# Performance work log

Measured on AMD Instinct MI355X. Metric: run time of the kernel, lower is better.

The kernel has to match this reference:

```python
import jax, jax.numpy as jnp
import numpy as np

D_MODEL, N_HEADS = 1024, 16
HEAD_DIM = D_MODEL // N_HEADS  # 64
BS, Q_LEN, SEQ_LEN = 4, 1024, 1024


def setup_inputs() -> dict:
    key = jax.random.key(0)
    kq, kk, kv, kp, km = jax.random.split(key, 5)
    q = jax.random.normal(kq, (BS, N_HEADS, Q_LEN, HEAD_DIM), dtype=jnp.float32)
    k = jax.random.normal(kk, (BS, N_HEADS, HEAD_DIM, SEQ_LEN), dtype=jnp.float32)
    v = jax.random.normal(kv, (BS, N_HEADS, SEQ_LEN, HEAD_DIM), dtype=jnp.float32)
    prev = jax.random.normal(kp, (BS, N_HEADS, Q_LEN, SEQ_LEN), dtype=jnp.float32)
    attn_weighted_mask = jax.random.uniform(km, (1, N_HEADS, Q_LEN, SEQ_LEN), dtype=jnp.float32)
    scale = jnp.asarray(HEAD_DIM ** (-0.5), dtype=jnp.float32)  # nn.Parameter scalar
    return {"q": q, "k": k, "v": v, "prev": prev,
            "attn_weighted_mask": attn_weighted_mask, "scale": scale}


def reference(q, k, v, prev, attn_weighted_mask, scale):
    # scores = (q @ k) * scale + prev       [bs, h, q_len, seq_len]
    attn_scores = jnp.einsum('bhqd,bhds->bhqs', q, k) * scale + prev
    # softmax over keys; attn_dropout p=0.0 -> identity
    attn_weights = jax.nn.softmax(attn_scores, axis=-1)
    # post-softmax elementwise weighted mask
    attn_weights = attn_weights * attn_weighted_mask
    # output = attn_weights @ v             [bs, h, q_len, d_v]
    output = jnp.einsum('bhqs,bhsd->bhqd', attn_weights, v)
    # res_attention=True -> also return weights and pre-softmax scores
    return output, attn_weights, attn_scores
```

## Files before the change

kernel.cpp:

```cpp
#include <hip/hip_runtime.h>
#include <hip/hip_bf16.h>


#define QL 1024
#define SL 1024
#define HD 64

typedef __attribute__((ext_vector_type(8))) short bf16x8;
typedef __attribute__((ext_vector_type(4))) float f32x4;

__device__ __forceinline__ short f2bf(float f) {
    union { float f; unsigned u; } v; v.f = f;
    unsigned r = v.u + 0x7FFFu + ((v.u >> 16) & 1u);
    return (short)(r >> 16);
}

__global__ __launch_bounds__(256) void
_ScaledDotProductAttention_Weighted_kernel(
    const float* __restrict__ q, const float* __restrict__ k,
    const float* __restrict__ v, const float* __restrict__ prev,
    const float* __restrict__ mask, const float* __restrict__ scale_p,
    float* __restrict__ out)
{
    const int WSTR = SL + 8;
    __shared__ short wbuf[16 * (SL + 8)];
    __shared__ float red[4 * 16];

    const int tid  = threadIdx.x;
    const int w    = tid >> 6;
    const int lane = tid & 63;
    const int quad = lane >> 4;
    const int lp   = lane & 15;

    const int blk = blockIdx.x;
    const int bh  = blk >> 6;
    const int qt  = blk & 63;
    const int h   = bh & 15;
    const int q0  = qt * 16;

    const float scale = scale_p[0];

    const float* Qb = q    + (size_t)bh * QL * HD + (size_t)q0 * HD;
    const float* Kb = k    + (size_t)bh * HD * SL;
    const float* Vb = v    + (size_t)bh * SL * HD;
    const float* Pb = prev + (size_t)bh * QL * SL + (size_t)q0 * SL;
    const float* Mb = mask + (size_t)h  * QL * SL + (size_t)q0 * SL;

    float* Ob   = out            + (size_t)bh * QL * HD + (size_t)q0 * HD;
    float* Wout = out + 4194304  + (size_t)bh * QL * SL + (size_t)q0 * SL;
    float* Sout = out + 71303168 + (size_t)bh * QL * SL + (size_t)q0 * SL;

    bf16x8 aq[2];
#pragma unroll
    for (int ks = 0; ks < 2; ++ks) {
        const float* qp = Qb + (size_t)lp * HD + ks * 32 + quad * 8;
#pragma unroll
        for (int j = 0; j < 8; ++j) aq[ks][j] = f2bf(qp[j] * scale);
    }

    const int s0 = 256 * w;
    f32x4 acc[16];
#pragma unroll
    for (int t = 0; t < 16; ++t) {
#pragma unroll
        for (int r = 0; r < 4; ++r)
            acc[t][r] = Pb[(size_t)(quad * 4 + r) * SL + s0 + 16 * t + lp];
    }
#pragma unroll
    for (int ks = 0; ks < 2; ++ks) {
#pragma unroll
        for (int t = 0; t < 16; ++t) {
            bf16x8 bk;
            const float* kp = Kb + (size_t)(ks * 32 + quad * 8) * SL + s0 + 16 * t + lp;
#pragma unroll
            for (int j = 0; j < 8; ++j) bk[j] = f2bf(kp[(size_t)j * SL]);
            acc[t] = __builtin_amdgcn_mfma_f32_16x16x32_bf16(aq[ks], bk, acc[t], 0, 0, 0);
        }
    }

    float lsum[4] = {0.f, 0.f, 0.f, 0.f};
#pragma unroll
    for (int t = 0; t < 16; ++t) {
#pragma unroll
        for (int r = 0; r < 4; ++r) {
            float sv = acc[t][r];
            Sout[(size_t)(quad * 4 + r) * SL + s0 + 16 * t + lp] = sv;
            float e = __expf(sv);
            acc[t][r] = e;
            lsum[r] += e;
        }
    }
#pragma unroll
    for (int r = 0; r < 4; ++r) {
        float s = lsum[r];
        s += __shfl_xor(s, 1);  s += __shfl_xor(s, 2);
        s += __shfl_xor(s, 4);  s += __shfl_xor(s, 8);
        lsum[r] = s;
    }
    if (lp == 0) {
#pragma unroll
        for (int r = 0; r < 4; ++r) red[w * 16 + quad * 4 + r] = lsum[r];
    }
    __syncthreads();
    float rinv[4];
#pragma unroll
    for (int r = 0; r < 4; ++r) {
        float s = red[0 * 16 + quad * 4 + r] + red[1 * 16 + quad * 4 + r]
                + red[2 * 16 + quad * 4 + r] + red[3 * 16 + quad * 4 + r];
        rinv[r] = 1.0f / s;
    }

#pragma unroll
    for (int t = 0; t < 16; ++t) {
#pragma unroll
        for (int r = 0; r < 4; ++r) {
            int row = quad * 4 + r;
            int col = s0 + 16 * t + lp;
            float wv = acc[t][r] * rinv[r] * Mb[(size_t)row * SL + col];
            Wout[(size_t)row * SL + col] = wv;
            wbuf[row * WSTR + col] = f2bf(wv);
        }
    }
    __syncthreads();

    f32x4 oacc = {0.f, 0.f, 0.f, 0.f};
#pragma unroll 4
    for (int ks = 0; ks < 32; ++ks) {
        bf16x8 aw = *(const bf16x8*)&wbuf[lp * WSTR + ks * 32 + quad * 8];
        bf16x8 bv;
        const float* vp = Vb + (size_t)(ks * 32 + quad * 8) * HD + 16 * w + lp;
#pragma unroll
        for (int j = 0; j < 8; ++j) bv[j] = f2bf(vp[(size_t)j * HD]);
        oacc = __builtin_amdgcn_mfma_f32_16x16x32_bf16(aw, bv, oacc, 0, 0, 0);
    }
#pragma unroll
    for (int r = 0; r < 4; ++r)
        Ob[(size_t)(quad * 4 + r) * HD + 16 * w + lp] = oacc[r];
}

extern "C" void kernel_launch(void* const* d_in, const int* in_sizes, int n_in,
                              void* d_out, int out_size, void* d_ws, size_t ws_size,
                              hipStream_t stream) {
    const float* q     = (const float*)d_in[0];
    const float* k     = (const float*)d_in[1];
    const float* v     = (const float*)d_in[2];
    const float* prev  = (const float*)d_in[3];
    const float* mask  = (const float*)d_in[4];
    const float* scale = (const float*)d_in[5];
    float* out = (float*)d_out;

    _ScaledDotProductAttention_Weighted_kernel<<<dim3(4096), dim3(256), 0, stream>>>(
        q, k, v, prev, mask, scale, out);
}
```

Baseline: 951.2 us.

## Prepack K and V to transposed bf16 in workspace before attention kernel

Adds a prepass kernel that converts K and V to bf16 and transposes them into the workspace, so the main kernel can do vectorized 16-byte loads instead of strided scalar fp32 loads with per-element conversion. The main kernel also drops the wbuf padding in favour of a blocked LDS layout, vectorizes the Q loads, adds prev after the MFMA instead of preloading it into the accumulators, and swizzles block order across 8 groups. A fallback path keeps the old kernel when the workspace is too small. The cost is an extra launch and extra global traffic for the prepacked copies, and a register/occupancy hint (launch_bounds 256,4).

```diff
diff --git a/kernel.cpp b/kernel.cpp
--- a/kernel.cpp
+++ b/kernel.cpp
@@ -1,5 +1,4 @@
 #include <hip/hip_runtime.h>
-#include <hip/hip_bf16.h>
 
 
 #define QL 1024
@@ -7,6 +6,7 @@
 #define HD 64
 
 typedef __attribute__((ext_vector_type(8))) short bf16x8;
+typedef __attribute__((ext_vector_type(4))) short bf16x4;
 typedef __attribute__((ext_vector_type(4))) float f32x4;
 
 __device__ __forceinline__ short f2bf(float f) {
@@ -15,8 +15,166 @@
     return (short)(r >> 16);
 }
 
-__global__ __launch_bounds__(256) void
-_ScaledDotProductAttention_Weighted_kernel(
+__global__ __launch_bounds__(256) void _prepack_kv(
+    const float* __restrict__ k, const float* __restrict__ v,
+    short* __restrict__ ws)
+{
+    __shared__ short tile[64][72];
+    const int t = threadIdx.x;
+    int b = blockIdx.x;
+    const float* src; short* dst; int ld_src, ld_dst;
+    if (b < 1024) {
+        const int bh = b >> 4, st = b & 15;
+        src = k + (size_t)bh * 65536 + st * 64;               ld_src = 1024;
+        dst = ws + (size_t)bh * 65536 + (size_t)st * 4096;    ld_dst = 64;
+    } else {
+        b -= 1024;
+        const int bh = b >> 4, st = b & 15;
+        src = v + (size_t)bh * 65536 + (size_t)st * 4096;     ld_src = 64;
+        dst = ws + 4194304 + (size_t)bh * 65536 + st * 64;    ld_dst = 1024;
+    }
+    {
+        const int r = t >> 2, c0 = (t & 3) * 16;
+#pragma unroll
+        for (int i = 0; i < 4; ++i) {
+            float4 f = *(const float4*)&src[(size_t)r * ld_src + c0 + 4 * i];
+            bf16x4 s4 = { f2bf(f.x), f2bf(f.y), f2bf(f.z), f2bf(f.w) };
+            *(bf16x4*)&tile[r][c0 + 4 * i] = s4;
+        }
+    }
+    __syncthreads();
+    {
+        const int r = t >> 2, c0 = (t & 3) * 16;
+        bf16x8 o0, o1;
+#pragma unroll
+        for (int j = 0; j < 8; ++j) o0[j] = tile[c0 + j][r];
+#pragma unroll
+        for (int j = 0; j < 8; ++j) o1[j] = tile[c0 + 8 + j][r];
+        *(bf16x8*)&dst[(size_t)r * ld_dst + c0]     = o0;
+        *(bf16x8*)&dst[(size_t)r * ld_dst + c0 + 8] = o1;
+    }
+}
+
+__global__ __launch_bounds__(256, 4) void _attn_main(
+    const float* __restrict__ q, const float* __restrict__ prev,
+    const float* __restrict__ mask, const float* __restrict__ scale_p,
+    const short* __restrict__ Kt, const short* __restrict__ Vt,
+    float* __restrict__ out)
+{
+    __shared__ short wbuf[16384];
+    __shared__ float red[64];
+
+    const int tid  = threadIdx.x;
+    const int w    = tid >> 6;
+    const int lane = tid & 63;
+    const int quad = lane >> 4;
+    const int lp   = lane & 15;
+
+    const int blk = (blockIdx.x & 7) * 512 + (blockIdx.x >> 3);
+    const int bh  = blk >> 6;
+    const int qt  = blk & 63;
+    const int h   = bh & 15;
+    const int q0  = qt * 16;
+
+    const float scale = scale_p[0];
+
+    const float* Qb = q    + (size_t)bh * QL * HD + (size_t)q0 * HD;
+    const float* Pb = prev + (size_t)bh * QL * SL + (size_t)q0 * SL;
+    const float* Mb = mask + (size_t)h  * QL * SL + (size_t)q0 * SL;
+    const short* Kb = Kt + (size_t)bh * (SL * HD);
+    const short* Vb = Vt + (size_t)bh * (SL * HD);
+
+    float* Ob   = out            + (size_t)bh * QL * HD + (size_t)q0 * HD;
+    float* Wout = out + 4194304  + (size_t)bh * QL * SL + (size_t)q0 * SL;
+    float* Sout = out + 71303168 + (size_t)bh * QL * SL + (size_t)q0 * SL;
+
+    bf16x8 aq[2];
+#pragma unroll
+    for (int ks = 0; ks < 2; ++ks) {
+        const float* qp = Qb + (size_t)lp * HD + ks * 32 + quad * 8;
+        float4 a = *(const float4*)qp;
+        float4 b = *(const float4*)(qp + 4);
+        aq[ks][0] = f2bf(a.x * scale); aq[ks][1] = f2bf(a.y * scale);
+        aq[ks][2] = f2bf(a.z * scale); aq[ks][3] = f2bf(a.w * scale);
+        aq[ks][4] = f2bf(b.x * scale); aq[ks][5] = f2bf(b.y * scale);
+        aq[ks][6] = f2bf(b.z * scale); aq[ks][7] = f2bf(b.w * scale);
+    }
+
+    const int s0 = 256 * w;
+    f32x4 acc[16];
+#pragma unroll
+    for (int t = 0; t < 16; ++t) acc[t] = (f32x4){0.f, 0.f, 0.f, 0.f};
+#pragma unroll
+    for (int ks = 0; ks < 2; ++ks) {
+#pragma unroll
+        for (int t = 0; t < 16; ++t) {
+            bf16x8 bk = *(const bf16x8*)&Kb[(size_t)(s0 + 16 * t + lp) * HD
+                                            + ks * 32 + quad * 8];
+            acc[t] = __builtin_amdgcn_mfma_f32_16x16x32_bf16(aq[ks], bk, acc[t], 0, 0, 0);
+        }
+    }
+
+    float lsum[4] = {0.f, 0.f, 0.f, 0.f};
+#pragma unroll
+    for (int t = 0; t < 16; ++t) {
+#pragma unroll
+        for (int r = 0; r < 4; ++r) {
+            const int row = quad * 4 + r;
+            const int col = s0 + 16 * t + lp;
+            float sv = acc[t][r] + Pb[(size_t)row * SL + col];
+            Sout[(size_t)row * SL + col] = sv;
+            float e = __expf(sv);
+            acc[t][r] = e;
+            lsum[r] += e;
+        }
+    }
+#pragma unroll
+    for (int r = 0; r < 4; ++r) {
+        float s = lsum[r];
+        s += __shfl_xor(s, 1);  s += __shfl_xor(s, 2);
+        s += __shfl_xor(s, 4);  s += __shfl_xor(s, 8);
+        lsum[r] = s;
+    }
+    if (lp == 0) {
+#pragma unroll
+        for (int r = 0; r < 4; ++r) red[w * 16 + quad * 4 + r] = lsum[r];
+    }
+    __syncthreads();
+    float rinv[4];
+#pragma unroll
+    for (int r = 0; r < 4; ++r) {
+        float s = red[0 * 16 + quad * 4 + r] + red[1 * 16 + quad * 4 + r]
+                + red[2 * 16 + quad * 4 + r] + red[3 * 16 + quad * 4 + r];
+        rinv[r] = 1.0f / s;
+    }
+
+#pragma unroll
+    for (int t = 0; t < 16; ++t) {
+#pragma unroll
+        for (int r = 0; r < 4; ++r) {
+            const int row = quad * 4 + r;
+            const int col = s0 + 16 * t + lp;
+            float wv = acc[t][r] * rinv[r] * Mb[(size_t)row * SL + col];
+            Wout[(size_t)row * SL + col] = wv;
+            wbuf[(((col >> 3) * 16) + row) * 8 + (lp & 7)] = f2bf(wv);
+        }
+    }
+    __syncthreads();
+
+    f32x4 oacc = {0.f, 0.f, 0.f, 0.f};
+#pragma unroll 4
+    for (int ks = 0; ks < 32; ++ks) {
+        bf16x8 aw = *(const bf16x8*)&wbuf[((ks * 4 + quad) * 16 + lp) * 8];
+        bf16x8 bv = *(const bf16x8*)&Vb[(size_t)(16 * w + lp) * SL
+                                        + ks * 32 + quad * 8];
+        oacc = __builtin_amdgcn_mfma_f32_16x16x32_bf16(aw, bv, oacc, 0, 0, 0);
+    }
+#pragma unroll
+    for (int r = 0; r < 4; ++r)
+        Ob[(size_t)(quad * 4 + r) * HD + 16 * w + lp] = oacc[r];
+}
+
+__global__ __launch_bounds__(256) void _attn_fallback(
     const float* __restrict__ q, const float* __restrict__ k,
     const float* __restrict__ v, const float* __restrict__ prev,
     const float* __restrict__ mask, const float* __restrict__ scale_p,
@@ -149,6 +307,13 @@
     const float* scale = (const float*)d_in[5];
     float* out = (float*)d_out;
 
-    _ScaledDotProductAttention_Weighted_kernel<<<dim3(4096), dim3(256), 0, stream>>>(
-        q, k, v, prev, mask, scale, out);
-}
+    if (d_ws != nullptr && ws_size >= (size_t)16 * 1024 * 1024) {
+        short* ws = (short*)d_ws;
+        _prepack_kv<<<dim3(2048), dim3(256), 0, stream>>>(k, v, ws);
+        _attn_main<<<dim3(4096), dim3(256), 0, stream>>>(
+            q, prev, mask, scale, ws, ws + 4194304, out);
+    } else {
+        _attn_fallback<<<dim3(4096), dim3(256), 0, stream>>>(
+            q, k, v, prev, mask, scale, out);
+    }
+}
```

Result: no change. 941.3 us (-1.0%).
